# Kernel tuning notes

Hardware: AMD Instinct MI355X
Metric: run time of the kernel (lower is better)

## Reference

```python
import jax, jax.numpy as jnp
import numpy as np

B, V, H, W = 2, 4, 352, 352
R_PIX = H * W
SH_DEGREE = 1
D_SH = (SH_DEGREE + 1) ** 2
SCALE_MIN, SCALE_MAX = 0.5, 15.0
EPS = 1e-8
C0 = 0.28209479177387814  # SH DC basis constant


def quat_to_mat(q):
    # (w, x, y, z) convention, matches pytorch3d quaternion_to_matrix
    w, x, y, z = q[..., 0], q[..., 1], q[..., 2], q[..., 3]
    two_s = 2.0 / jnp.sum(q * q, axis=-1)
    o = jnp.stack([
        1 - two_s * (y * y + z * z), two_s * (x * y - z * w), two_s * (x * z + y * w),
        two_s * (x * y + z * w), 1 - two_s * (x * x + z * z), two_s * (y * z - x * w),
        two_s * (x * z - y * w), two_s * (y * z + x * w), 1 - two_s * (x * x + y * y),
    ], axis=-1)
    return o.reshape(*q.shape[:-1], 3, 3)


def setup_inputs() -> dict:
    key = jax.random.key(0)
    ks = jax.random.split(key, 8)
    # valid c2w extrinsics: random rotation (from unit quaternion) + translation
    q = jax.random.normal(ks[0], (B, V, 4))
    q = q / jnp.linalg.norm(q, axis=-1, keepdims=True)
    Rm = quat_to_mat(q)
    t = jax.random.normal(ks[1], (B, V, 3))
    E = jnp.zeros((B, V, 4, 4))
    E = E.at[..., :3, :3].set(Rm).at[..., :3, 3].set(t).at[..., 3, 3].set(1.0)
    extrinsics = E.reshape(B, V, 1, 1, 1, 4, 4)
    # normalized pinhole intrinsics
    f = jax.random.uniform(ks[2], (B, V, 2), minval=0.8, maxval=1.2)
    K = jnp.zeros((B, V, 3, 3))
    K = K.at[..., 0, 0].set(f[..., 0]).at[..., 1, 1].set(f[..., 1])
    K = K.at[..., 0, 2].set(0.5).at[..., 1, 2].set(0.5).at[..., 2, 2].set(1.0)
    intrinsics = K.reshape(B, V, 1, 1, 1, 3, 3)
    coordinates = jax.random.uniform(ks[3], (B, V, R_PIX, 1, 1, 2))
    depths = jax.random.uniform(ks[4], (B, V, R_PIX, 1, 1), minval=0.5, maxval=10.0)
    opacities = jax.random.uniform(ks[5], (B, V, R_PIX, 1, 1))
    raw_gaussians = jax.random.normal(ks[6], (B, V, R_PIX, 1, 1, 7 + 3 * D_SH))
    input_images = jax.random.uniform(ks[7], (B, V, 3, H, W))
    sh_mask = jnp.ones((D_SH,), jnp.float32)
    for deg in range(1, SH_DEGREE + 1):
        sh_mask = sh_mask.at[deg ** 2:(deg + 1) ** 2].set(0.1 * 0.25 ** deg)
    return {"extrinsics": extrinsics, "intrinsics": intrinsics, "coordinates": coordinates,
            "depths": depths, "opacities": opacities, "raw_gaussians": raw_gaussians,
            "input_images": input_images, "sh_mask": sh_mask}


def reference(extrinsics, intrinsics, coordinates, depths, opacities, raw_gaussians, input_images, sh_mask):
    d_sh = sh_mask.shape[0]
    # split raw gaussians: scales (3), quaternion (4), sh (3*d_sh)
    scales = jnp.clip(jax.nn.softplus(raw_gaussians[..., :3] - 4.0), SCALE_MIN, SCALE_MAX)
    rot = raw_gaussians[..., 3:7]
    rotations = rot / (jnp.linalg.norm(rot, axis=-1, keepdims=True) + EPS)
    sh = raw_gaussians[..., 7:].reshape(*raw_gaussians.shape[:-1], 3, d_sh) * sh_mask
    # inject image colors into the DC SH coefficient
    b, v, c, h, w = input_images.shape
    imgs = input_images.transpose(0, 1, 3, 4, 2).reshape(b, v, h * w, 1, 1, c)
    sh = sh.at[..., 0].add((imgs - 0.5) / C0)  # RGB2SH
    # covariance = R diag(s^2) R^T, then rotate into world frame
    Rq = quat_to_mat(rotations)
    cov = jnp.einsum('...ij,...j,...kj->...ik', Rq, scales * scales, Rq)
    Rc = extrinsics[..., :3, :3]  # (b,v,1,1,1,3,3) c2w rotation
    cov = jnp.einsum('...ij,...jk,...lk->...il', Rc, cov, Rc)
    # unproject rays: d = normalize(K^-1 [x,y,1]), world dir = R d, origin = t
    Kinv = jnp.linalg.inv(intrinsics)
    xy1 = jnp.concatenate([coordinates, jnp.ones_like(coordinates[..., :1])], axis=-1)
    d = jnp.einsum('...ij,...j->...i', Kinv, xy1)
    d = d / jnp.linalg.norm(d, axis=-1, keepdims=True)
    dirs = jnp.einsum('...ij,...j->...i', Rc, d)
    means = jnp.broadcast_to(extrinsics[..., :3, 3], dirs.shape) + dirs * depths[..., None]
    # rotate SH: degree 0 identity; degree 1 Wigner-D = P R P^T with P: (x,y,z)->(y,z,x)
    perm = jnp.array([1, 2, 0])
    D1 = Rc[..., perm[:, None], perm[None, :]]  # (b,v,1,1,1,3,3)
    sh1 = jnp.einsum('...ij,...xj->...xi', D1, sh[..., 1:4])
    harmonics = jnp.concatenate([sh[..., :1], sh1], axis=-1)
    return means, cov, scales, rotations, harmonics, opacities
```

## Files before the change

kernel.cpp:

```cpp
#include <hip/hip_runtime.h>

#define R_PIX 123904
#define NVIEW 8
#define NPIX  (R_PIX * (size_t)NVIEW)

#define OFF_MEANS  ((size_t)0)
#define OFF_COV    ((size_t)(3  * NPIX))
#define OFF_SCALES ((size_t)(12 * NPIX))
#define OFF_ROT    ((size_t)(15 * NPIX))
#define OFF_HARM   ((size_t)(19 * NPIX))
#define OFF_OPAC   ((size_t)(31 * NPIX))

#define LDS_DW   4864
#define MEANS_L  0
#define COV_L    768
#define SCALES_L 3072
#define HARM_L   0

typedef float f4v __attribute__((ext_vector_type(4)));

__device__ __forceinline__ void nt_store4(float* p, float x, float y, float z, float w) {
    f4v v = { x, y, z, w };
    __builtin_nontemporal_store(v, (f4v*)p);
}
__device__ __forceinline__ void nt_store4(float* p, const float4& v) {
    nt_store4(p, v.x, v.y, v.z, v.w);
}

__device__ __forceinline__ void g2lds16(const void* g, void* l) {
    __builtin_amdgcn_global_load_lds(
        (__attribute__((address_space(1))) void*)g,
        (__attribute__((address_space(3))) void*)l,
        16, 0, 0);
}

__global__ __launch_bounds__(256) void gaussian_adapter_kernel(
    const float* __restrict__ extr,
    const float* __restrict__ intr,
    const float* __restrict__ coords,
    const float* __restrict__ depths,
    const float* __restrict__ opac,
    const float* __restrict__ raw,
    const float* __restrict__ imgs,
    const float* __restrict__ shmask,
    float* __restrict__ out)
{
    const int t   = threadIdx.x;
    const int bv  = blockIdx.y;
    const int bp0 = blockIdx.x * 256;
    const size_t base_pix = (size_t)bv * R_PIX + bp0;
    const int p   = bp0 + t;
    const size_t pix = base_pix + t;

    __shared__ __align__(16) float lds[LDS_DW];

    {
        const float4* g = (const float4*)(raw + base_pix * 19);
        float4* s = (float4*)lds;
        const int wave = t >> 6;
        #pragma unroll
        for (int i = 0; i < 4; i++)
            g2lds16(g + i * 256 + t, s + i * 256 + wave * 64);
        if (t < 192)
            g2lds16(g + 1024 + t, s + 1024 + wave * 64);
    }

    float Rc[3][3], tvec[3];
    {
        const float* E = extr + bv * 16;
        #pragma unroll
        for (int i = 0; i < 3; i++) {
            #pragma unroll
            for (int j = 0; j < 3; j++) Rc[i][j] = E[i * 4 + j];
            tvec[i] = E[i * 4 + 3];
        }
    }
    const float* K = intr + bv * 9;
    const float fx = K[0], cx = K[2];
    const float fy = K[4], cy = K[5];
    const float sm0 = shmask[0], sm1 = shmask[1], sm2 = shmask[2], sm3 = shmask[3];

    const float2 uv  = ((const float2*)coords)[pix];
    const float  dep = depths[pix];
    const float  op  = opac[pix];
    float im[3];
    #pragma unroll
    for (int c = 0; c < 3; c++)
        im[c] = imgs[((size_t)bv * 3 + c) * R_PIX + p];

    __syncthreads();

    const float* my = lds + t * 19;

    float sc[3];
    #pragma unroll
    for (int k = 0; k < 3; k++) {
        float xv = my[k] - 4.0f;
        float sp = fmaxf(xv, 0.0f) + log1pf(expf(-fabsf(xv)));
        sc[k] = fminf(fmaxf(sp, 0.5f), 15.0f);
    }

    float q0 = my[3], q1 = my[4], q2 = my[5], q3 = my[6];
    {
        const float qn = q0 * q0 + q1 * q1 + q2 * q2 + q3 * q3;
        const float inorm = 1.0f / (sqrtf(qn) + 1e-8f);
        q0 *= inorm; q1 *= inorm; q2 *= inorm; q3 *= inorm;
    }

    const float two_s = 2.0f / (q0 * q0 + q1 * q1 + q2 * q2 + q3 * q3);
    float Rq[3][3];
    Rq[0][0] = 1.0f - two_s * (q2 * q2 + q3 * q3);
    Rq[0][1] = two_s * (q1 * q2 - q3 * q0);
    Rq[0][2] = two_s * (q1 * q3 + q2 * q0);
    Rq[1][0] = two_s * (q1 * q2 + q3 * q0);
    Rq[1][1] = 1.0f - two_s * (q1 * q1 + q3 * q3);
    Rq[1][2] = two_s * (q2 * q3 - q1 * q0);
    Rq[2][0] = two_s * (q1 * q3 - q2 * q0);
    Rq[2][1] = two_s * (q2 * q3 + q1 * q0);
    Rq[2][2] = 1.0f - two_s * (q1 * q1 + q2 * q2);

    const float s2[3] = { sc[0] * sc[0], sc[1] * sc[1], sc[2] * sc[2] };
    float cov3[3][3];
    #pragma unroll
    for (int i = 0; i < 3; i++)
        #pragma unroll
        for (int k = 0; k < 3; k++)
            cov3[i][k] = Rq[i][0] * s2[0] * Rq[k][0]
                       + Rq[i][1] * s2[1] * Rq[k][1]
                       + Rq[i][2] * s2[2] * Rq[k][2];
    float cov[3][3];
    #pragma unroll
    for (int i = 0; i < 3; i++) {
        float m0 = Rc[i][0] * cov3[0][0] + Rc[i][1] * cov3[1][0] + Rc[i][2] * cov3[2][0];
        float m1 = Rc[i][0] * cov3[0][1] + Rc[i][1] * cov3[1][1] + Rc[i][2] * cov3[2][1];
        float m2 = Rc[i][0] * cov3[0][2] + Rc[i][1] * cov3[1][2] + Rc[i][2] * cov3[2][2];
        #pragma unroll
        for (int l = 0; l < 3; l++)
            cov[i][l] = m0 * Rc[l][0] + m1 * Rc[l][1] + m2 * Rc[l][2];
    }

    float means[3];
    {
        float d0 = (uv.x - cx) / fx;
        float d1 = (uv.y - cy) / fy;
        float d2 = 1.0f;
        const float rn = 1.0f / sqrtf(d0 * d0 + d1 * d1 + d2 * d2);
        d0 *= rn; d1 *= rn; d2 *= rn;
        #pragma unroll
        for (int i = 0; i < 3; i++)
            means[i] = tvec[i] + (Rc[i][0] * d0 + Rc[i][1] * d1 + Rc[i][2] * d2) * dep;
    }

    float harm[3][4];
    {
        const float invC0 = 1.0f / 0.28209479177387814f;
        const int perm[3] = {1, 2, 0};
        #pragma unroll
        for (int c = 0; c < 3; c++) {
            float s1  = my[7 + c * 4 + 1] * sm1;
            float s2v = my[7 + c * 4 + 2] * sm2;
            float s3  = my[7 + c * 4 + 3] * sm3;
            harm[c][0] = my[7 + c * 4] * sm0 + (im[c] - 0.5f) * invC0;
            #pragma unroll
            for (int i = 0; i < 3; i++)
                harm[c][1 + i] = Rc[perm[i]][perm[0]] * s1
                               + Rc[perm[i]][perm[1]] * s2v
                               + Rc[perm[i]][perm[2]] * s3;
        }
    }

    __syncthreads();

    #pragma unroll
    for (int i = 0; i < 3; i++) lds[MEANS_L + t * 3 + i] = means[i];
    #pragma unroll
    for (int i = 0; i < 3; i++)
        #pragma unroll
        for (int j = 0; j < 3; j++) lds[COV_L + t * 9 + i * 3 + j] = cov[i][j];
    #pragma unroll
    for (int i = 0; i < 3; i++) lds[SCALES_L + t * 3 + i] = sc[i];

    __syncthreads();

    float4 mA  = make_float4(0.f, 0.f, 0.f, 0.f);
    float4 sA  = make_float4(0.f, 0.f, 0.f, 0.f);
    float4 cv2 = make_float4(0.f, 0.f, 0.f, 0.f);
    const float4 cv0 = ((const float4*)(lds + COV_L))[t];
    const float4 cv1 = ((const float4*)(lds + COV_L))[t + 256];
    if (t < 64)  cv2 = ((const float4*)(lds + COV_L))[t + 512];
    if (t < 192) {
        mA = ((const float4*)(lds + MEANS_L))[t];
        sA = ((const float4*)(lds + SCALES_L))[t];
    }

    __syncthreads();

    #pragma unroll
    for (int c = 0; c < 3; c++)
        #pragma unroll
        for (int j = 0; j < 4; j++) lds[HARM_L + t * 13 + c * 4 + j] = harm[c][j];

    __syncthreads();

    float4 hv[3];
    #pragma unroll
    for (int it = 0; it < 3; it++) {
        const int i = t + 256 * it;
        const int px = i / 3, k = i % 3;
        const float* s = lds + HARM_L + px * 13 + k * 4;
        hv[it] = make_float4(s[0], s[1], s[2], s[3]);
    }

    nt_store4(out + OFF_ROT + pix * 4, q0, q1, q2, q3);
    __builtin_nontemporal_store(op, out + OFF_OPAC + pix);
    {
        float* g = out + OFF_MEANS + base_pix * 3;
        if (t < 192) nt_store4(g + t * 4, mA);
    }
    {
        float* g = out + OFF_COV + base_pix * 9;
        nt_store4(g + t * 4, cv0);
        nt_store4(g + (t + 256) * 4, cv1);
        if (t < 64) nt_store4(g + (t + 512) * 4, cv2);
    }
    {
        float* g = out + OFF_SCALES + base_pix * 3;
        if (t < 192) nt_store4(g + t * 4, sA);
    }
    {
        float* g = out + OFF_HARM + base_pix * 12;
        #pragma unroll
        for (int it = 0; it < 3; it++)
            nt_store4(g + (t + 256 * it) * 4, hv[it]);
    }
}

extern "C" void kernel_launch(void* const* d_in, const int* in_sizes, int n_in,
                              void* d_out, int out_size, void* d_ws, size_t ws_size,
                              hipStream_t stream) {
    const float* extr   = (const float*)d_in[0];
    const float* intr   = (const float*)d_in[1];
    const float* coords = (const float*)d_in[2];
    const float* depths = (const float*)d_in[3];
    const float* opac   = (const float*)d_in[4];
    const float* raw    = (const float*)d_in[5];
    const float* imgs   = (const float*)d_in[6];
    const float* shmask = (const float*)d_in[7];
    float* out = (float*)d_out;

    dim3 grid(R_PIX / 256, NVIEW);
    dim3 block(256);
    gaussian_adapter_kernel<<<grid, block, 0, stream>>>(
        extr, intr, coords, depths, opac, raw, imgs, shmask, out);
}
```

Before: 224.6 us.

## Use per-wave LDS slices for output transposes and switch to fast-math intrinsics

After: 223.4 us. Within noise of the previous version (-0.5%).

```diff
diff --git a/kernel.cpp b/kernel.cpp
--- a/kernel.cpp
+++ b/kernel.cpp
@@ -11,11 +11,8 @@
 #define OFF_HARM   ((size_t)(19 * NPIX))
 #define OFF_OPAC   ((size_t)(31 * NPIX))
 
-#define LDS_DW   4864
-#define MEANS_L  0
-#define COV_L    768
-#define SCALES_L 3072
-#define HARM_L   0
+#define SLICE_DW 1216
+#define LDS_DW   (SLICE_DW * 4)
 
 typedef float f4v __attribute__((ext_vector_type(4)));
 
@@ -32,6 +29,10 @@
         (__attribute__((address_space(1))) void*)g,
         (__attribute__((address_space(3))) void*)l,
         16, 0, 0);
+}
+
+__device__ __forceinline__ void lds_fence() {
+    asm volatile("s_waitcnt lgkmcnt(0)" ::: "memory");
 }
 
 __global__ __launch_bounds__(256) void gaussian_adapter_kernel(
@@ -45,24 +46,24 @@
     const float* __restrict__ shmask,
     float* __restrict__ out)
 {
-    const int t   = threadIdx.x;
-    const int bv  = blockIdx.y;
-    const int bp0 = blockIdx.x * 256;
+    const int t    = threadIdx.x;
+    const int lane = t & 63;
+    const int w    = t >> 6;
+    const int bv   = blockIdx.y;
+    const int bp0  = blockIdx.x * 256;
     const size_t base_pix = (size_t)bv * R_PIX + bp0;
     const int p   = bp0 + t;
     const size_t pix = base_pix + t;
 
     __shared__ __align__(16) float lds[LDS_DW];
-
-    {
-        const float4* g = (const float4*)(raw + base_pix * 19);
-        float4* s = (float4*)lds;
-        const int wave = t >> 6;
-        #pragma unroll
-        for (int i = 0; i < 4; i++)
-            g2lds16(g + i * 256 + t, s + i * 256 + wave * 64);
-        if (t < 192)
-            g2lds16(g + 1024 + t, s + 1024 + wave * 64);
+    float* slice = lds + w * SLICE_DW;
+
+    {
+        const float4* g = (const float4*)(raw + base_pix * 19) + w * 304;
+        #pragma unroll
+        for (int r = 0; r < 4; r++)
+            g2lds16(g + r * 64 + lane, (char*)slice + r * 1024);
+        g2lds16(g + 240 + lane, (char*)slice + 3840);
     }
 
     float Rc[3][3], tvec[3];
@@ -92,22 +93,29 @@
 
     const float* my = lds + t * 19;
 
+    float rg[19];
+    #pragma unroll
+    for (int i = 0; i < 19; i++) rg[i] = my[i];
+
+    const float LOG2E = 1.4426950408889634f;
+    const float LN2   = 0.6931471805599453f;
     float sc[3];
     #pragma unroll
     for (int k = 0; k < 3; k++) {
-        float xv = my[k] - 4.0f;
-        float sp = fmaxf(xv, 0.0f) + log1pf(expf(-fabsf(xv)));
+        float xv = rg[k] - 4.0f;
+        float e  = __builtin_amdgcn_exp2f(-fabsf(xv) * LOG2E);
+        float sp = fmaxf(xv, 0.0f) + LN2 * __builtin_amdgcn_logf(1.0f + e);
         sc[k] = fminf(fmaxf(sp, 0.5f), 15.0f);
     }
 
-    float q0 = my[3], q1 = my[4], q2 = my[5], q3 = my[6];
+    float q0 = rg[3], q1 = rg[4], q2 = rg[5], q3 = rg[6];
     {
         const float qn = q0 * q0 + q1 * q1 + q2 * q2 + q3 * q3;
-        const float inorm = 1.0f / (sqrtf(qn) + 1e-8f);
+        const float inorm = __builtin_amdgcn_rsqf(qn);
         q0 *= inorm; q1 *= inorm; q2 *= inorm; q3 *= inorm;
     }
 
-    const float two_s = 2.0f / (q0 * q0 + q1 * q1 + q2 * q2 + q3 * q3);
+    const float two_s = 2.0f;
     float Rq[3][3];
     Rq[0][0] = 1.0f - two_s * (q2 * q2 + q3 * q3);
     Rq[0][1] = two_s * (q1 * q2 - q3 * q0);
@@ -141,11 +149,13 @@
 
     float means[3];
     {
-        float d0 = (uv.x - cx) / fx;
-        float d1 = (uv.y - cy) / fy;
-        float d2 = 1.0f;
-        const float rn = 1.0f / sqrtf(d0 * d0 + d1 * d1 + d2 * d2);
-        d0 *= rn; d1 *= rn; d2 *= rn;
+        const float rfx = __builtin_amdgcn_rcpf(fx);
+        const float rfy = __builtin_amdgcn_rcpf(fy);
+        float d0 = (uv.x - cx) * rfx;
+        float d1 = (uv.y - cy) * rfy;
+        const float rn = __builtin_amdgcn_rsqf(d0 * d0 + d1 * d1 + 1.0f);
+        d0 *= rn; d1 *= rn;
+        const float d2 = rn;
         #pragma unroll
         for (int i = 0; i < 3; i++)
             means[i] = tvec[i] + (Rc[i][0] * d0 + Rc[i][1] * d1 + Rc[i][2] * d2) * dep;
@@ -157,10 +167,10 @@
         const int perm[3] = {1, 2, 0};
         #pragma unroll
         for (int c = 0; c < 3; c++) {
-            float s1  = my[7 + c * 4 + 1] * sm1;
-            float s2v = my[7 + c * 4 + 2] * sm2;
-            float s3  = my[7 + c * 4 + 3] * sm3;
-            harm[c][0] = my[7 + c * 4] * sm0 + (im[c] - 0.5f) * invC0;
+            float s1  = rg[7 + c * 4 + 1] * sm1;
+            float s2v = rg[7 + c * 4 + 2] * sm2;
+            float s3  = rg[7 + c * 4 + 3] * sm3;
+            harm[c][0] = rg[7 + c * 4] * sm0 + (im[c] - 0.5f) * invC0;
             #pragma unroll
             for (int i = 0; i < 3; i++)
                 harm[c][1 + i] = Rc[perm[i]][perm[0]] * s1
@@ -169,69 +179,56 @@
         }
     }
 
-    __syncthreads();
-
-    #pragma unroll
-    for (int i = 0; i < 3; i++) lds[MEANS_L + t * 3 + i] = means[i];
-    #pragma unroll
-    for (int i = 0; i < 3; i++)
-        #pragma unroll
-        for (int j = 0; j < 3; j++) lds[COV_L + t * 9 + i * 3 + j] = cov[i][j];
-    #pragma unroll
-    for (int i = 0; i < 3; i++) lds[SCALES_L + t * 3 + i] = sc[i];
-
-    __syncthreads();
-
-    float4 mA  = make_float4(0.f, 0.f, 0.f, 0.f);
-    float4 sA  = make_float4(0.f, 0.f, 0.f, 0.f);
-    float4 cv2 = make_float4(0.f, 0.f, 0.f, 0.f);
-    const float4 cv0 = ((const float4*)(lds + COV_L))[t];
-    const float4 cv1 = ((const float4*)(lds + COV_L))[t + 256];
-    if (t < 64)  cv2 = ((const float4*)(lds + COV_L))[t + 512];
-    if (t < 192) {
-        mA = ((const float4*)(lds + MEANS_L))[t];
-        sA = ((const float4*)(lds + SCALES_L))[t];
-    }
-
-    __syncthreads();
-
-    #pragma unroll
-    for (int c = 0; c < 3; c++)
-        #pragma unroll
-        for (int j = 0; j < 4; j++) lds[HARM_L + t * 13 + c * 4 + j] = harm[c][j];
-
-    __syncthreads();
-
-    float4 hv[3];
-    #pragma unroll
-    for (int it = 0; it < 3; it++) {
-        const int i = t + 256 * it;
-        const int px = i / 3, k = i % 3;
-        const float* s = lds + HARM_L + px * 13 + k * 4;
-        hv[it] = make_float4(s[0], s[1], s[2], s[3]);
-    }
-
     nt_store4(out + OFF_ROT + pix * 4, q0, q1, q2, q3);
     __builtin_nontemporal_store(op, out + OFF_OPAC + pix);
-    {
-        float* g = out + OFF_MEANS + base_pix * 3;
-        if (t < 192) nt_store4(g + t * 4, mA);
-    }
-    {
-        float* g = out + OFF_COV + base_pix * 9;
-        nt_store4(g + t * 4, cv0);
-        nt_store4(g + (t + 256) * 4, cv1);
-        if (t < 64) nt_store4(g + (t + 512) * 4, cv2);
-    }
-    {
-        float* g = out + OFF_SCALES + base_pix * 3;
-        if (t < 192) nt_store4(g + t * 4, sA);
-    }
-    {
-        float* g = out + OFF_HARM + base_pix * 12;
-        #pragma unroll
-        for (int it = 0; it < 3; it++)
-            nt_store4(g + (t + 256 * it) * 4, hv[it]);
+
+    const size_t wpix = base_pix + (size_t)(w * 64);
+    float* means_g = out + OFF_MEANS  + wpix * 3;
+    float* cov_g   = out + OFF_COV    + wpix * 9;
+    float* sc_g    = out + OFF_SCALES + wpix * 3;
+    float* hm_g    = out + OFF_HARM   + wpix * 12;
+
+    lds_fence();
+    #pragma unroll
+    for (int i = 0; i < 3; i++) slice[lane * 3 + i] = means[i];
+    #pragma unroll
+    for (int i = 0; i < 3; i++)
+        #pragma unroll
+        for (int j = 0; j < 3; j++) slice[192 + lane * 9 + i * 3 + j] = cov[i][j];
+    #pragma unroll
+    for (int i = 0; i < 3; i++) slice[768 + lane * 3 + i] = sc[i];
+
+    lds_fence();
+
+    {
+        const float4* sv = (const float4*)slice;
+        float4 v0 = sv[lane];
+        if (lane < 48) nt_store4(means_g + 4 * lane, v0);
+        else           nt_store4(cov_g + 4 * (lane - 48), v0);
+        float4 v1 = sv[lane + 64];
+        nt_store4(cov_g + 4 * (lane + 16), v1);
+        float4 v2 = sv[lane + 128];
+        nt_store4(cov_g + 4 * (lane + 80), v2);
+        if (lane < 48) {
+            float4 v3 = sv[lane + 192];
+            nt_store4(sc_g + 4 * lane, v3);
+        }
+    }
+
+    lds_fence();
+    #pragma unroll
+    for (int c = 0; c < 3; c++)
+        #pragma unroll
+        for (int j = 0; j < 4; j++) slice[lane * 13 + c * 4 + j] = harm[c][j];
+
+    lds_fence();
+
+    #pragma unroll
+    for (int it = 0; it < 3; it++) {
+        const int i = lane + 64 * it;
+        const int px = i / 3, k = i % 3;
+        const float* s = slice + px * 13 + k * 4;
+        nt_store4(hm_g + 4 * i, s[0], s[1], s[2], s[3]);
     }
 }
 
```
